# Optimization experiments

Hardware: AMD Instinct MI355X
Metric: run time of the kernel (lower is better)

Reference implementation:

```python
import jax, jax.numpy as jnp
import numpy as np

B, N, D = 8, 65536, 192
EPS = 1e-5  # matches cal_norm_batch eps

# corner offsets (i,j,k) in {0,1}^3, shape [2,2,2,3]
_OFFS = np.stack(np.meshgrid(np.arange(2), np.arange(2), np.arange(2), indexing='ij'), -1)


def setup_inputs() -> dict:
    key = jax.random.key(0)
    k1, k2 = jax.random.split(key)
    pss = jax.random.uniform(k1, (B, 3, N), jnp.float32)          # points in [0,1]^3
    sdf_grids = jax.random.normal(k2, (B, D, D, D), jnp.float32)  # per-batch SDF grids
    first = jnp.zeros((B, 3), jnp.float32)                        # grid origin
    coef = jnp.full((B, 3), float(D - 2), jnp.float32)            # 1/voxel_size
    max_limit = jnp.full((B, 3), float(D - 2), jnp.float32)       # keeps idx+1 <= D-1
    return {"pss": pss, "sdf_grids": sdf_grids, "first": first, "coef": coef, "max_limit": max_limit}


def reference(pss, sdf_grids, first, coef, max_limit):
    p = jnp.transpose(pss, (0, 2, 1))  # [B,N,3]
    f_full = jnp.clip(jnp.minimum((p - first[:, None, :]) * coef[:, None, :],
                                  max_limit[:, None, :]), 0.0)
    base = jnp.floor(f_full)
    frac = f_full - base               # [B,N,3] trilinear fractions
    idx8 = base.astype(jnp.int32)[:, :, None, None, None, :] + jnp.asarray(_OFFS, jnp.int32)  # [B,N,2,2,2,3]
    # 8-corner gather, per-batch grid
    corners = jax.vmap(lambda g, I: g[I[..., 0], I[..., 1], I[..., 2]])(sdf_grids, idx8)  # [B,N,2,2,2]
    fx, fy, fz = frac[..., 0], frac[..., 1], frac[..., 2]
    wx = jnp.stack([1 - fx, fx], -1)  # [B,N,2]
    wy = jnp.stack([1 - fy, fy], -1)
    wz = jnp.stack([1 - fz, fz], -1)
    # trilinear SDF value
    dss = jnp.einsum('bnijk,bni,bnj,bnk->bn', corners, wx, wy, wz)
    # finite-difference normals (interp3d_batch with grad=True along each axis)
    n_z = jnp.einsum('bnij,bni,bnj->bn', corners[..., 1] - corners[..., 0], wx, wy)
    n_y = jnp.einsum('bnik,bni,bnk->bn', corners[:, :, :, 1, :] - corners[:, :, :, 0, :], wx, wz)
    n_x = jnp.einsum('bnjk,bnj,bnk->bn', corners[:, :, 1] - corners[:, :, 0], wy, wz)
    n = jnp.stack([n_x, n_y, n_z], -1)  # [B,N,3]
    nss = n / jnp.clip(jnp.linalg.norm(n, axis=-1, keepdims=True), EPS)
    loss = -jnp.sum(jnp.minimum(dss, 0.0))
    return dss, nss, loss
```

## Files before the change

### kernel.cpp

```cpp
#include <hip/hip_runtime.h>

#define BB 8
#define NN 65536
#define DD 192
#define EPSV 1e-5f


__global__ __launch_bounds__(256) void tri_sdf_kernel(
    const float* __restrict__ pss,
    const float* __restrict__ grid,
    const float* __restrict__ first,
    const float* __restrict__ coef,
    const float* __restrict__ maxl,
    float* __restrict__ dss,
    float* __restrict__ nss,
    float* __restrict__ loss)
{
    const int t = blockIdx.x * blockDim.x + threadIdx.x;
    const int b = t >> 16;
    const int n = t & (NN - 1);

    const float* pb = pss + (size_t)b * 3 * NN + n;
    const float px = pb[0];
    const float py = pb[NN];
    const float pz = pb[2 * NN];

    const float fx_full = fmaxf(fminf((px - first[3*b+0]) * coef[3*b+0], maxl[3*b+0]), 0.0f);
    const float fy_full = fmaxf(fminf((py - first[3*b+1]) * coef[3*b+1], maxl[3*b+1]), 0.0f);
    const float fz_full = fmaxf(fminf((pz - first[3*b+2]) * coef[3*b+2], maxl[3*b+2]), 0.0f);

    const int bx = (int)floorf(fx_full);
    const int by = (int)floorf(fy_full);
    const int bz = (int)floorf(fz_full);
    const float fx = fx_full - (float)bx;
    const float fy = fy_full - (float)by;
    const float fz = fz_full - (float)bz;

    const float* g = grid + (size_t)b * DD * DD * DD
                          + ((size_t)bx * DD + by) * DD + bz;
    const float c000 = g[0];
    const float c001 = g[1];
    const float c010 = g[DD];
    const float c011 = g[DD + 1];
    const float c100 = g[DD * DD];
    const float c101 = g[DD * DD + 1];
    const float c110 = g[DD * DD + DD];
    const float c111 = g[DD * DD + DD + 1];

    const float wx0 = 1.0f - fx, wx1 = fx;
    const float wy0 = 1.0f - fy, wy1 = fy;
    const float wz0 = 1.0f - fz, wz1 = fz;

    const float d00 = wz0 * c000 + wz1 * c001;
    const float d01 = wz0 * c010 + wz1 * c011;
    const float d10 = wz0 * c100 + wz1 * c101;
    const float d11 = wz0 * c110 + wz1 * c111;
    const float d0  = wy0 * d00 + wy1 * d01;
    const float d1  = wy0 * d10 + wy1 * d11;
    const float dv  = wx0 * d0 + wx1 * d1;

    const float nz = wx0 * (wy0 * (c001 - c000) + wy1 * (c011 - c010))
                   + wx1 * (wy0 * (c101 - c100) + wy1 * (c111 - c110));
    const float ny = wx0 * (wz0 * (c010 - c000) + wz1 * (c011 - c001))
                   + wx1 * (wz0 * (c110 - c100) + wz1 * (c111 - c101));
    const float nx = wy0 * (wz0 * (c100 - c000) + wz1 * (c101 - c001))
                   + wy1 * (wz0 * (c110 - c010) + wz1 * (c111 - c011));

    const float nrm = sqrtf(nx * nx + ny * ny + nz * nz);
    const float inv = 1.0f / fmaxf(nrm, EPSV);

    dss[t] = dv;
    float* np_ = nss + (size_t)t * 3;
    np_[0] = nx * inv;
    np_[1] = ny * inv;
    np_[2] = nz * inv;

    float lp = fminf(dv, 0.0f);
    #pragma unroll
    for (int off = 32; off > 0; off >>= 1)
        lp += __shfl_down(lp, off, 64);
    if ((threadIdx.x & 63) == 0)
        atomicAdd(loss, -lp);
}

extern "C" void kernel_launch(void* const* d_in, const int* in_sizes, int n_in,
                              void* d_out, int out_size, void* d_ws, size_t ws_size,
                              hipStream_t stream) {
    const float* pss   = (const float*)d_in[0];
    const float* grid  = (const float*)d_in[1];
    const float* first = (const float*)d_in[2];
    const float* coef  = (const float*)d_in[3];
    const float* maxl  = (const float*)d_in[4];

    float* out  = (float*)d_out;
    float* dss  = out;
    float* nss  = out + (size_t)BB * NN;
    float* loss = out + (size_t)4 * BB * NN;

    hipMemsetAsync(loss, 0, sizeof(float), stream);

    const int threads = 256;
    const int blocks  = (BB * NN) / threads;
    tri_sdf_kernel<<<blocks, threads, 0, stream>>>(pss, grid, first, coef, maxl,
                                                   dss, nss, loss);
}
```

Measured before the change: 367.7 us.

## Bin points by spatial cell with counting sort before trilinear gather

Adds a counting sort of points into 8x8x8-voxel cells: a histogram pass, a three-stage prefix scan, and a scatter that writes fractions, packed base indices and original ids. The main kernel then runs over the sorted points, so neighbouring threads gather nearby grid voxels, which is meant to improve cache locality on the 8-corner random gathers. Outputs are written back to their original indices through a scatter, and the loss atomics are cut to one per block using a shared-memory reduction. The cost is five extra kernel launches, atomics on the histogram, and extra workspace traffic.

```diff
diff --git a/kernel.cpp b/kernel.cpp
--- a/kernel.cpp
+++ b/kernel.cpp
@@ -5,36 +5,131 @@
 #define DD 192
 #define EPSV 1e-5f
 
-
-__global__ __launch_bounds__(256) void tri_sdf_kernel(
-    const float* __restrict__ pss,
-    const float* __restrict__ grid,
-    const float* __restrict__ first,
-    const float* __restrict__ coef,
-    const float* __restrict__ maxl,
-    float* __restrict__ dss,
-    float* __restrict__ nss,
-    float* __restrict__ loss)
-{
-    const int t = blockIdx.x * blockDim.x + threadIdx.x;
-    const int b = t >> 16;
+#define CAX 24
+#define CELLS_B (CAX * CAX * CAX)
+#define TCELLS (BB * CELLS_B)
+#define NPTS (BB * NN)
+#define SCAN_BLOCKS (TCELLS / 256)
+
+#define SORT0 (TCELLS + 512)
+
+__device__ __forceinline__ void point_setup(
+    const float* __restrict__ pss, const float* __restrict__ first,
+    const float* __restrict__ coef, const float* __restrict__ maxl,
+    int t, int& b, float& fx, float& fy, float& fz,
+    int& bx, int& by, int& bz, int& key)
+{
+    b = t >> 16;
     const int n = t & (NN - 1);
-
     const float* pb = pss + (size_t)b * 3 * NN + n;
     const float px = pb[0];
     const float py = pb[NN];
     const float pz = pb[2 * NN];
 
-    const float fx_full = fmaxf(fminf((px - first[3*b+0]) * coef[3*b+0], maxl[3*b+0]), 0.0f);
-    const float fy_full = fmaxf(fminf((py - first[3*b+1]) * coef[3*b+1], maxl[3*b+1]), 0.0f);
-    const float fz_full = fmaxf(fminf((pz - first[3*b+2]) * coef[3*b+2], maxl[3*b+2]), 0.0f);
-
-    const int bx = (int)floorf(fx_full);
-    const int by = (int)floorf(fy_full);
-    const int bz = (int)floorf(fz_full);
-    const float fx = fx_full - (float)bx;
-    const float fy = fy_full - (float)by;
-    const float fz = fz_full - (float)bz;
+    const float Fx = fmaxf(fminf((px - first[3*b+0]) * coef[3*b+0], maxl[3*b+0]), 0.0f);
+    const float Fy = fmaxf(fminf((py - first[3*b+1]) * coef[3*b+1], maxl[3*b+1]), 0.0f);
+    const float Fz = fmaxf(fminf((pz - first[3*b+2]) * coef[3*b+2], maxl[3*b+2]), 0.0f);
+
+    bx = (int)floorf(Fx);
+    by = (int)floorf(Fy);
+    bz = (int)floorf(Fz);
+    fx = Fx - (float)bx;
+    fy = Fy - (float)by;
+    fz = Fz - (float)bz;
+
+    key = ((b * CAX + (bx >> 3)) * CAX + (by >> 3)) * CAX + (bz >> 3);
+}
+
+__global__ __launch_bounds__(256) void hist_kernel(
+    const float* __restrict__ pss, const float* __restrict__ first,
+    const float* __restrict__ coef, const float* __restrict__ maxl,
+    unsigned* __restrict__ hist)
+{
+    const int t = blockIdx.x * blockDim.x + threadIdx.x;
+    int b, bx, by, bz, key; float fx, fy, fz;
+    point_setup(pss, first, coef, maxl, t, b, fx, fy, fz, bx, by, bz, key);
+    atomicAdd(&hist[key], 1u);
+}
+
+__global__ __launch_bounds__(256) void scan1_kernel(unsigned* __restrict__ hist,
+                                                    unsigned* __restrict__ bsum)
+{
+    __shared__ unsigned s[256];
+    const int tid = threadIdx.x;
+    const int i = blockIdx.x * 256 + tid;
+    const unsigned v = hist[i];
+    s[tid] = v;
+    __syncthreads();
+    #pragma unroll
+    for (int off = 1; off < 256; off <<= 1) {
+        unsigned tv = (tid >= off) ? s[tid - off] : 0u;
+        __syncthreads();
+        s[tid] += tv;
+        __syncthreads();
+    }
+    hist[i] = s[tid] - v;
+    if (tid == 255) bsum[blockIdx.x] = s[255];
+}
+
+__global__ __launch_bounds__(512) void scan2_kernel(unsigned* __restrict__ bsum)
+{
+    __shared__ unsigned s[512];
+    const int tid = threadIdx.x;
+    const unsigned v = (tid < SCAN_BLOCKS) ? bsum[tid] : 0u;
+    s[tid] = v;
+    __syncthreads();
+    #pragma unroll
+    for (int off = 1; off < 512; off <<= 1) {
+        unsigned tv = (tid >= off) ? s[tid - off] : 0u;
+        __syncthreads();
+        s[tid] += tv;
+        __syncthreads();
+    }
+    if (tid < SCAN_BLOCKS) bsum[tid] = s[tid] - v;
+}
+
+__global__ __launch_bounds__(256) void scan3_kernel(unsigned* __restrict__ hist,
+                                                    const unsigned* __restrict__ bsum)
+{
+    const int i = blockIdx.x * 256 + threadIdx.x;
+    hist[i] += bsum[blockIdx.x];
+}
+
+__global__ __launch_bounds__(256) void scatter_kernel(
+    const float* __restrict__ pss, const float* __restrict__ first,
+    const float* __restrict__ coef, const float* __restrict__ maxl,
+    unsigned* __restrict__ cursor,
+    float* __restrict__ sfx, float* __restrict__ sfy, float* __restrict__ sfz,
+    unsigned* __restrict__ sbase, unsigned* __restrict__ sorig)
+{
+    const int t = blockIdx.x * blockDim.x + threadIdx.x;
+    int b, bx, by, bz, key; float fx, fy, fz;
+    point_setup(pss, first, coef, maxl, t, b, fx, fy, fz, bx, by, bz, key);
+    const unsigned pos = atomicAdd(&cursor[key], 1u);
+    sfx[pos] = fx;
+    sfy[pos] = fy;
+    sfz[pos] = fz;
+    sbase[pos] = ((unsigned)b << 24) | ((unsigned)bx << 16) | ((unsigned)by << 8) | (unsigned)bz;
+    sorig[pos] = (unsigned)t;
+}
+
+__global__ __launch_bounds__(256) void main_kernel(
+    const float* __restrict__ grid,
+    const float* __restrict__ sfx, const float* __restrict__ sfy,
+    const float* __restrict__ sfz, const unsigned* __restrict__ sbase,
+    const unsigned* __restrict__ sorig,
+    float* __restrict__ dss, float* __restrict__ nss, float* __restrict__ loss)
+{
+    const int i = blockIdx.x * blockDim.x + threadIdx.x;
+
+    const float fx = sfx[i];
+    const float fy = sfy[i];
+    const float fz = sfz[i];
+    const unsigned pk = sbase[i];
+    const int b  = (int)(pk >> 24);
+    const int bx = (int)((pk >> 16) & 255u);
+    const int by = (int)((pk >> 8) & 255u);
+    const int bz = (int)(pk & 255u);
 
     const float* g = grid + (size_t)b * DD * DD * DD
                           + ((size_t)bx * DD + by) * DD + bz;
@@ -69,6 +164,7 @@
     const float nrm = sqrtf(nx * nx + ny * ny + nz * nz);
     const float inv = 1.0f / fmaxf(nrm, EPSV);
 
+    const unsigned t = sorig[i];
     dss[t] = dv;
     float* np_ = nss + (size_t)t * 3;
     np_[0] = nx * inv;
@@ -79,8 +175,12 @@
     #pragma unroll
     for (int off = 32; off > 0; off >>= 1)
         lp += __shfl_down(lp, off, 64);
-    if ((threadIdx.x & 63) == 0)
-        atomicAdd(loss, -lp);
+    __shared__ float wsum[4];
+    const int wid = threadIdx.x >> 6;
+    if ((threadIdx.x & 63) == 0) wsum[wid] = lp;
+    __syncthreads();
+    if (threadIdx.x == 0)
+        atomicAdd(loss, -(wsum[0] + wsum[1] + wsum[2] + wsum[3]));
 }
 
 extern "C" void kernel_launch(void* const* d_in, const int* in_sizes, int n_in,
@@ -97,10 +197,27 @@
     float* nss  = out + (size_t)BB * NN;
     float* loss = out + (size_t)4 * BB * NN;
 
+    unsigned* ws    = (unsigned*)d_ws;
+    unsigned* hist  = ws;
+    unsigned* bsum  = ws + TCELLS;
+    float*    sfx   = (float*)(ws + SORT0 + (size_t)0 * NPTS);
+    float*    sfy   = (float*)(ws + SORT0 + (size_t)1 * NPTS);
+    float*    sfz   = (float*)(ws + SORT0 + (size_t)2 * NPTS);
+    unsigned* sbase =          ws + SORT0 + (size_t)3 * NPTS;
+    unsigned* sorig =          ws + SORT0 + (size_t)4 * NPTS;
+
+    hipMemsetAsync(hist, 0, (size_t)TCELLS * sizeof(unsigned), stream);
     hipMemsetAsync(loss, 0, sizeof(float), stream);
 
     const int threads = 256;
-    const int blocks  = (BB * NN) / threads;
-    tri_sdf_kernel<<<blocks, threads, 0, stream>>>(pss, grid, first, coef, maxl,
-                                                   dss, nss, loss);
-}
+    const int pblocks = NPTS / threads;
+
+    hist_kernel<<<pblocks, threads, 0, stream>>>(pss, first, coef, maxl, hist);
+    scan1_kernel<<<SCAN_BLOCKS, 256, 0, stream>>>(hist, bsum);
+    scan2_kernel<<<1, 512, 0, stream>>>(bsum);
+    scan3_kernel<<<SCAN_BLOCKS, 256, 0, stream>>>(hist, bsum);
+    scatter_kernel<<<pblocks, threads, 0, stream>>>(pss, first, coef, maxl, hist,
+                                                    sfx, sfy, sfz, sbase, sorig);
+    main_kernel<<<pblocks, threads, 0, stream>>>(grid, sfx, sfy, sfz, sbase, sorig,
+                                                 dss, nss, loss);
+}
```

New measurement: 376.7 us. +2.5%, slower.
